# Performance work log

Measured on AMD Instinct MI355X. Metric: run time of the kernel, lower is better.

The kernel has to match this reference:

```python
import jax, jax.numpy as jnp
import numpy as np

B, S, D, H = 4, 2048, 1024, 16
HD = D // H          # head_dim = 64; per-head scale = sqrt(HD) as in source
FF = 4096
EPS = 1e-5


def _layernorm(x, g, b):
    m = jnp.mean(x, axis=-1, keepdims=True)
    v = jnp.mean(jnp.square(x - m), axis=-1, keepdims=True)
    return (x - m) * jax.lax.rsqrt(v + EPS) * g + b


def setup_inputs() -> dict:
    key = jax.random.key(0)
    ks = jax.random.split(key, 10)
    std = 0.02
    return {
        "x": jax.random.normal(ks[0], (B, S, D), jnp.float32),
        "wq": jax.random.normal(ks[1], (H, D, HD), jnp.float32) * std,
        "bq": jnp.zeros((H, HD), jnp.float32),
        "wk": jax.random.normal(ks[2], (H, D, HD), jnp.float32) * std,
        "bk": jnp.zeros((H, HD), jnp.float32),
        "wv": jax.random.normal(ks[3], (H, D, HD), jnp.float32) * std,
        "bv": jnp.zeros((H, HD), jnp.float32),
        "wo": jax.random.normal(ks[4], (D, D), jnp.float32) * std,
        "bo": jnp.zeros((D,), jnp.float32),
        "w1": jax.random.normal(ks[5], (D, FF), jnp.float32) * std,
        "b1": jnp.zeros((FF,), jnp.float32),
        "w2": jax.random.normal(ks[6], (FF, D), jnp.float32) * std,
        "b2": jnp.zeros((D,), jnp.float32),
        "g1": jnp.ones((D,), jnp.float32),
        "beta1": jnp.zeros((D,), jnp.float32),
        "g2": jnp.ones((D,), jnp.float32),
        "beta2": jnp.zeros((D,), jnp.float32),
    }


def reference(x, wq, bq, wk, bk, wv, bv, wo, bo, w1, b1, w2, b2, g1, beta1, g2, beta2):
    # Per-head Q/K/V projections (stacked over heads) -> [B,H,S,HD]
    q = jnp.einsum('bsd,hdf->bhsf', x, wq) + bq[None, :, None, :]
    k = jnp.einsum('bsd,hdf->bhsf', x, wk) + bk[None, :, None, :]
    v = jnp.einsum('bsd,hdf->bhsf', x, wv) + bv[None, :, None, :]

    scale = jnp.sqrt(jnp.asarray(HD, jnp.float32))
    att = jnp.einsum('bhqf,bhkf->bhqk', q, k) / scale  # [B,H,S,S]
    causal = jnp.tril(jnp.ones((S, S), dtype=bool))
    att = jnp.where(causal[None, None], att, -jnp.inf)
    p = jax.nn.softmax(att, axis=-1)
    o = jnp.einsum('bhqk,bhkf->bhqf', p, v)            # [B,H,S,HD]
    o = o.transpose(0, 2, 1, 3).reshape(B, S, D)       # concat heads
    attn_out = o @ wo + bo

    h = _layernorm(x + attn_out, g1, beta1)            # post-LN, dropout=0 (eval)
    ff = jax.nn.gelu(h @ w1 + b1, approximate=False) @ w2 + b2
    return _layernorm(h + ff, g2, beta2)
```

## Files before the change

### kernel.cpp

```cpp
#include <hip/hip_runtime.h>
#include <hip/hip_bf16.h>
#include <math.h>

typedef __bf16 bf16x8 __attribute__((ext_vector_type(8)));
typedef float floatx4 __attribute__((ext_vector_type(4)));
typedef unsigned short ushort8 __attribute__((ext_vector_type(8)));
typedef unsigned short ushort4v __attribute__((ext_vector_type(4)));

__device__ __forceinline__ unsigned short f2bs(float f){
  union { float f; unsigned u; } v; v.f = f;
  unsigned r = v.u + 0x7fffu + ((v.u >> 16) & 1u);
  return (unsigned short)(r >> 16);
}

__device__ __forceinline__ unsigned pk2(float a, float b){
  union { __hip_bfloat162 h; unsigned u; } cv;
  cv.h = __float22bfloat162_rn(make_float2(a, b));
  return cv.u;
}

__device__ __forceinline__ void gl_lds16(const void* g, void* l){
  __builtin_amdgcn_global_load_lds(
      (const __attribute__((address_space(1))) void*)g,
      (__attribute__((address_space(3))) void*)l,
      16, 0, 0);
}

__global__ __launch_bounds__(256) void cvt_x(const float* __restrict__ x,
                                             unsigned short* __restrict__ o){
  const int i = (blockIdx.x*256 + threadIdx.x)*4;
  const float4 v = *(const float4*)(x + i);
  ushort4v u = { f2bs(v.x), f2bs(v.y), f2bs(v.z), f2bs(v.w) };
  *(ushort4v*)(o + i) = u;
}

__global__ __launch_bounds__(256) void transpose_pack(const float* __restrict__ src,
                                                      unsigned short* __restrict__ dst,
                                                      int R, int C){
  __shared__ float tile[32][65];
  const int r0 = blockIdx.y*32, c0 = blockIdx.x*64;
  const int t = threadIdx.x;
  {
    const int r = t >> 3, cc = (t & 7)*8;
    const float* p = src + (size_t)(r0+r)*C + c0 + cc;
    const float4 v0 = *(const float4*)p;
    const float4 v1 = *(const float4*)(p+4);
    tile[r][cc+0]=v0.x; tile[r][cc+1]=v0.y; tile[r][cc+2]=v0.z; tile[r][cc+3]=v0.w;
    tile[r][cc+4]=v1.x; tile[r][cc+5]=v1.y; tile[r][cc+6]=v1.z; tile[r][cc+7]=v1.w;
  }
  __syncthreads();
  const int f = t >> 2, rr = (t & 3)*8;
  ushort8 u;
  #pragma unroll
  for (int j=0;j<8;j++) u[j] = f2bs(tile[rr+j][f]);
  *(ushort8*)(dst + (size_t)(c0+f)*R + r0 + rr) = u;
}

__global__ __launch_bounds__(256) void pack_qkv(const float* __restrict__ wq,
                                                const float* __restrict__ wk,
                                                const float* __restrict__ wv,
                                                const float* __restrict__ bq,
                                                const float* __restrict__ bk,
                                                const float* __restrict__ bv,
                                                unsigned short* __restrict__ Wt,
                                                float* __restrict__ Bc){
  __shared__ float tile[32][65];
  const int dt = blockIdx.x, h = blockIdx.y, sel = blockIdx.z;
  const float* src = (sel==0 ? wq : (sel==1 ? wk : wv)) + (size_t)h*65536;
  const int t = threadIdx.x, d0 = dt*32;
  {
    const int r = t >> 3, cc = (t & 7)*8;
    const float* p = src + (size_t)(d0+r)*64 + cc;
    const float4 v0 = *(const float4*)p;
    const float4 v1 = *(const float4*)(p+4);
    tile[r][cc+0]=v0.x; tile[r][cc+1]=v0.y; tile[r][cc+2]=v0.z; tile[r][cc+3]=v0.w;
    tile[r][cc+4]=v1.x; tile[r][cc+5]=v1.y; tile[r][cc+6]=v1.z; tile[r][cc+7]=v1.w;
  }
  __syncthreads();
  const int f = t >> 2, rr = (t & 3)*8;
  ushort8 u;
  #pragma unroll
  for (int j=0;j<8;j++) u[j] = f2bs(tile[rr+j][f]);
  const size_t n = (size_t)sel*1024 + h*64 + f;
  *(ushort8*)(Wt + n*1024 + d0 + rr) = u;
  if (dt==0 && t<64){
    const float* bs = (sel==0 ? bq : (sel==1 ? bk : bv)) + h*64;
    Bc[sel*1024 + h*64 + t] = bs[t];
  }
}

template<int MODE>
__global__ __launch_bounds__(256) void gemm_bt(const unsigned short* __restrict__ A,
                                               const unsigned short* __restrict__ Bt,
                                               const float* __restrict__ bias,
                                               void* __restrict__ out0,
                                               void* __restrict__ out1,
                                               void* __restrict__ out2,
                                               int M, int N, int K){
  __shared__ __align__(16) unsigned short As[128*64];
  __shared__ __align__(16) unsigned short Bs[128*64];
  const int tid = threadIdx.x;
  const int wave = tid >> 6, lane = tid & 63;
  const int quad = lane >> 4, l15 = lane & 15;
  const int lin = blockIdx.x;
  const int xcd = lin & 7, rest = lin >> 3;
  const int mloc = rest & 7, nt = rest >> 3;
  const int m0 = (xcd*8 + mloc) << 7, n0 = nt << 7;
  const int wr = (wave >> 1) << 6, wc = (wave & 1) << 6;

  floatx4 acc[4][4];
  #pragma unroll
  for (int i=0;i<4;i++)
    #pragma unroll
    for (int j=0;j<4;j++) acc[i][j] = (floatx4)0.0f;

  const unsigned short* gA[4];
  const unsigned short* gB[4];
  int ldsOff[4];
  #pragma unroll
  for (int r2=0;r2<4;r2++){
    const int slot = r2*256 + wave*64 + lane;
    const int row = slot >> 3, ch = slot & 7;
    const int col = (ch ^ (row & 7))*8;
    gA[r2] = A  + (size_t)(m0 + row)*K + col;
    gB[r2] = Bt + (size_t)(n0 + row)*K + col;
    ldsOff[r2] = slot*8;
  }
  const int cs0 = (quad ^ (l15 & 7))*8;
  const int cs1 = ((4 + quad) ^ (l15 & 7))*8;

  for (int k0 = 0; k0 < K; k0 += 64){
    #pragma unroll
    for (int r2=0;r2<4;r2++){
      gl_lds16(gA[r2] + k0, As + ldsOff[r2]);
      gl_lds16(gB[r2] + k0, Bs + ldsOff[r2]);
    }
    __syncthreads();
    #pragma unroll
    for (int ks=0;ks<2;ks++){
      const int cs = ks ? cs1 : cs0;
      bf16x8 af[4], bfv[4];
      #pragma unroll
      for (int t=0;t<4;t++){
        af[t]  = *(const bf16x8*)(As + (wr + t*16 + l15)*64 + cs);
        bfv[t] = *(const bf16x8*)(Bs + (wc + t*16 + l15)*64 + cs);
      }
      #pragma unroll
      for (int i=0;i<4;i++)
        #pragma unroll
        for (int j=0;j<4;j++)
          acc[i][j] = __builtin_amdgcn_mfma_f32_16x16x32_bf16(af[i], bfv[j], acc[i][j], 0,0,0);
    }
    __syncthreads();
  }

  #pragma unroll
  for (int i=0;i<4;i++){
    #pragma unroll
    for (int j=0;j<4;j++){
      const int col = n0 + wc + j*16 + l15;
      const float bsv = bias[col];
      if (MODE == 3 && col >= 2048){
        const int n = col - 2048, h = n >> 6, fidx = n & 63;
        const int rowb = m0 + wr + i*16 + quad*4;
        const int b = rowb >> 11, s = rowb & 2047;
        float v0 = acc[i][j][0] + bsv, v1 = acc[i][j][1] + bsv;
        float v2 = acc[i][j][2] + bsv, v3 = acc[i][j][3] + bsv;
        uint2 pkd = make_uint2(pk2(v0, v1), pk2(v2, v3));
        *(uint2*)((unsigned short*)out2 + (size_t)(((b<<4) + h)*64 + fidx)*2048 + s) = pkd;
        continue;
      }
      #pragma unroll
      for (int r=0;r<4;r++){
        const int row = m0 + wr + i*16 + quad*4 + r;
        const float v = acc[i][j][r] + bsv;
        if (MODE == 1){
          ((float*)out0)[(size_t)row*N + col] = v;
        } else if (MODE == 2){
          const float u = 0.7978845608f*v*(1.0f + 0.044715f*v*v);
          const float e = __builtin_amdgcn_exp2f(u * 2.885390082f);
          const float th = 1.0f - 2.0f/(1.0f + e);
          const float gl = 0.5f*v*(1.0f + th);
          ((unsigned short*)out0)[(size_t)row*N + col] = f2bs(gl);
        } else {
          if (col < 1024){
            ((unsigned short*)out0)[(size_t)row*1024 + col] = f2bs(v*0.18033688011112042f);
          } else {
            ((unsigned short*)out1)[(size_t)row*1024 + (col-1024)] = f2bs(v);
          }
        }
      }
    }
  }
}

__global__ __launch_bounds__(256, 4) void attn(const unsigned short* __restrict__ Q,
                                               const unsigned short* __restrict__ Kg,
                                               const unsigned short* __restrict__ Vt,
                                               unsigned short* __restrict__ O){
  __shared__ __align__(16) unsigned short Ks[64*64];
  __shared__ __align__(16) unsigned short Vs[64*64];
  __shared__ __align__(16) unsigned short PT[4][16*68];

  const int qt_lo = blockIdx.x;
  const int qt_hi = 31 - qt_lo;
  const int bh = blockIdx.y;
  const int b = bh >> 4, h = bh & 15;
  const int tid = threadIdx.x, wave = tid >> 6, lane = tid & 63;
  const int quad = lane >> 4, l15 = lane & 15;

  const size_t qbase = (size_t)((b<<11) + (wave<<4) + l15)*1024 + (h<<6);
  bf16x8 qf_hi[2], qf_lo[2];
  qf_hi[0] = *(const bf16x8*)(Q + qbase + (size_t)(qt_hi<<6)*1024 + quad*8);
  qf_hi[1] = *(const bf16x8*)(Q + qbase + (size_t)(qt_hi<<6)*1024 + 32 + quad*8);
  qf_lo[0] = *(const bf16x8*)(Q + qbase + (size_t)(qt_lo<<6)*1024 + quad*8);
  qf_lo[1] = *(const bf16x8*)(Q + qbase + (size_t)(qt_lo<<6)*1024 + 32 + quad*8);

  floatx4 oa_hi[4], oa_lo[4];
  #pragma unroll
  for (int i=0;i<4;i++){ oa_hi[i] = (floatx4)0.0f; oa_lo[i] = (floatx4)0.0f; }
  float mi_hi = -3e38f, li_hi = 0.0f;
  float mi_lo = -3e38f, li_lo = 0.0f;

  const unsigned short* Kbh = Kg + ((size_t)(b<<11))*1024 + (h<<6);
  const unsigned short* Vbh = Vt + (size_t)bh*64*2048;
  unsigned short* Pw = &PT[wave][0];

  const int slot0 = wave*128 + lane;
  const int krow0 = slot0 >> 3, kc0 = (slot0 & 7) ^ (krow0 & 7);
  const int slot1 = slot0 + 64;
  const int krow1 = slot1 >> 3, kc1 = (slot1 & 7) ^ (krow1 & 7);

  auto tile_step = [&](const bf16x8* qf, floatx4* oa, float& mi, float& li, bool diag){
    floatx4 sa[4];
    #pragma unroll
    for (int tj=0;tj<4;tj++){
      sa[tj] = (floatx4)0.0f;
      #pragma unroll
      for (int ks=0;ks<2;ks++){
        const int n = tj*16 + l15;
        const int c = (ks*4 + quad) ^ (n & 7);
        const bf16x8 kf = *(const bf16x8*)(Ks + n*64 + c*8);
        sa[tj] = __builtin_amdgcn_mfma_f32_16x16x32_bf16(kf, qf[ks], sa[tj], 0,0,0);
      }
    }
    if (diag){
      const int qrow = (wave<<4) + l15;
      #pragma unroll
      for (int tj=0;tj<4;tj++)
        #pragma unroll
        for (int r=0;r<4;r++)
          if (tj*16 + quad*4 + r > qrow) sa[tj][r] = -1e30f;
    }
    float mx = fmaxf(fmaxf(fmaxf(sa[0][0],sa[0][1]),fmaxf(sa[0][2],sa[0][3])),
                     fmaxf(fmaxf(sa[1][0],sa[1][1]),fmaxf(sa[1][2],sa[1][3])));
    mx = fmaxf(mx, fmaxf(fmaxf(fmaxf(sa[2][0],sa[2][1]),fmaxf(sa[2][2],sa[2][3])),
                         fmaxf(fmaxf(sa[3][0],sa[3][1]),fmaxf(sa[3][2],sa[3][3]))));
    mx = fmaxf(mx, __shfl_xor(mx, 16, 64));
    mx = fmaxf(mx, __shfl_xor(mx, 32, 64));
    const float mn = fmaxf(mi, mx);
    const float al = __builtin_amdgcn_exp2f(mi - mn);
    float rs = 0.0f;
    #pragma unroll
    for (int tj=0;tj<4;tj++)
      #pragma unroll
      for (int r=0;r<4;r++){
        const float p = __builtin_amdgcn_exp2f(sa[tj][r] - mn);
        sa[tj][r] = p;
        rs += p;
      }
    rs += __shfl_xor(rs, 16, 64);
    rs += __shfl_xor(rs, 32, 64);
    li = li*al + rs;
    mi = mn;
    #pragma unroll
    for (int tn=0;tn<4;tn++) oa[tn] *= al;

    #pragma unroll
    for (int tj=0;tj<4;tj++){
      uint2 pkd = make_uint2(pk2(sa[tj][0], sa[tj][1]), pk2(sa[tj][2], sa[tj][3]));
      *(uint2*)(Pw + l15*68 + tj*16 + quad*4) = pkd;
    }
    #pragma unroll
    for (int ks2=0;ks2<2;ks2++){
      const bf16x8 pf = *(const bf16x8*)(Pw + l15*68 + ks2*32 + quad*8);
      #pragma unroll
      for (int tn=0;tn<4;tn++){
        const int n2 = tn*16 + l15;
        const int c = (ks2*4 + quad) ^ (n2 & 7);
        const bf16x8 vf = *(const bf16x8*)(Vs + n2*64 + c*8);
        oa[tn] = __builtin_amdgcn_mfma_f32_16x16x32_bf16(vf, pf, oa[tn], 0,0,0);
      }
    }
  };

  for (int kt = 0; kt <= qt_hi; ++kt){
    gl_lds16(Kbh + (size_t)((kt<<6) + krow0)*1024 + kc0*8, Ks + wave*1024);
    gl_lds16(Kbh + (size_t)((kt<<6) + krow1)*1024 + kc1*8, Ks + wave*1024 + 512);
    gl_lds16(Vbh + (size_t)krow0*2048 + (kt<<6) + kc0*8, Vs + wave*1024);
    gl_lds16(Vbh + (size_t)krow1*2048 + (kt<<6) + kc1*8, Vs + wave*1024 + 512);
    __syncthreads();

    tile_step(qf_hi, oa_hi, mi_hi, li_hi, kt == qt_hi);
    if (kt <= qt_lo)
      tile_step(qf_lo, oa_lo, mi_lo, li_lo, kt == qt_lo);

    __syncthreads();
  }

  {
    const float inv = 1.0f / li_hi;
    unsigned short* Orow = O + (size_t)((b<<11) + (qt_hi<<6) + (wave<<4) + l15)*1024 + (h<<6);
    #pragma unroll
    for (int tn=0;tn<4;tn++){
      uint2 pkd = make_uint2(pk2(oa_hi[tn][0]*inv, oa_hi[tn][1]*inv),
                             pk2(oa_hi[tn][2]*inv, oa_hi[tn][3]*inv));
      *(uint2*)(Orow + tn*16 + quad*4) = pkd;
    }
  }
  {
    const float inv = 1.0f / li_lo;
    unsigned short* Orow = O + (size_t)((b<<11) + (qt_lo<<6) + (wave<<4) + l15)*1024 + (h<<6);
    #pragma unroll
    for (int tn=0;tn<4;tn++){
      uint2 pkd = make_uint2(pk2(oa_lo[tn][0]*inv, oa_lo[tn][1]*inv),
                             pk2(oa_lo[tn][2]*inv, oa_lo[tn][3]*inv));
      *(uint2*)(Orow + tn*16 + quad*4) = pkd;
    }
  }
}

__global__ __launch_bounds__(256) void ln_res(const float* __restrict__ a,
                                              const float* __restrict__ bsrc,
                                              const float* __restrict__ g,
                                              const float* __restrict__ be,
                                              float* __restrict__ of,
                                              unsigned short* __restrict__ ob){
  __shared__ float red1[4], red2[4];
  const int row = blockIdx.x, t = threadIdx.x;
  const int wave = t >> 6, lane = t & 63;
  const float4 va = *(const float4*)(a + (size_t)row*1024 + t*4);
  const float4 vb = *(const float4*)(bsrc + (size_t)row*1024 + t*4);
  float xs[4] = {va.x+vb.x, va.y+vb.y, va.z+vb.z, va.w+vb.w};
  float s = xs[0]+xs[1]+xs[2]+xs[3];
  #pragma unroll
  for (int d=1; d<64; d<<=1) s += __shfl_xor(s, d, 64);
  if (lane==0) red1[wave] = s;
  __syncthreads();
  const float mean = (red1[0]+red1[1]+red1[2]+red1[3]) * (1.0f/1024.0f);
  float vsum = 0.0f;
  #pragma unroll
  for (int i=0;i<4;i++){ const float d = xs[i]-mean; vsum += d*d; }
  #pragma unroll
  for (int d=1; d<64; d<<=1) vsum += __shfl_xor(vsum, d, 64);
  if (lane==0) red2[wave] = vsum;
  __syncthreads();
  const float var = (red2[0]+red2[1]+red2[2]+red2[3]) * (1.0f/1024.0f);
  const float rs = rsqrtf(var + 1e-5f);
  const float4 gg = *(const float4*)(g + t*4);
  const float4 bb = *(const float4*)(be + t*4);
  float y[4];
  y[0] = (xs[0]-mean)*rs*gg.x + bb.x;
  y[1] = (xs[1]-mean)*rs*gg.y + bb.y;
  y[2] = (xs[2]-mean)*rs*gg.z + bb.z;
  y[3] = (xs[3]-mean)*rs*gg.w + bb.w;
  if (of){
    float4 o4; o4.x=y[0]; o4.y=y[1]; o4.z=y[2]; o4.w=y[3];
    *(float4*)(of + (size_t)row*1024 + t*4) = o4;
  }
  if (ob){
    ushort4v u = { f2bs(y[0]), f2bs(y[1]), f2bs(y[2]), f2bs(y[3]) };
    *(ushort4v*)(ob + (size_t)row*1024 + t*4) = u;
  }
}

extern "C" void kernel_launch(void* const* d_in, const int* in_sizes, int n_in,
                              void* d_out, int out_size, void* d_ws, size_t ws_size,
                              hipStream_t stream){
  (void)in_sizes; (void)n_in; (void)out_size; (void)ws_size;
  const float* x  = (const float*)d_in[0];
  const float* wq = (const float*)d_in[1];
  const float* bq = (const float*)d_in[2];
  const float* wk = (const float*)d_in[3];
  const float* bk = (const float*)d_in[4];
  const float* wv = (const float*)d_in[5];
  const float* bv = (const float*)d_in[6];
  const float* wo = (const float*)d_in[7];
  const float* bo = (const float*)d_in[8];
  const float* w1 = (const float*)d_in[9];
  const float* b1 = (const float*)d_in[10];
  const float* w2 = (const float*)d_in[11];
  const float* b2 = (const float*)d_in[12];
  const float* g1 = (const float*)d_in[13];
  const float* be1= (const float*)d_in[14];
  const float* g2 = (const float*)d_in[15];
  const float* be2= (const float*)d_in[16];
  float* out = (float*)d_out;

  char* ws = (char*)d_ws;
  size_t off = 0;
  auto take = [&](size_t bytes)->char*{
    char* p = ws + off; off += (bytes + 255) & ~(size_t)255; return p;
  };
  unsigned short* Xb  = (unsigned short*)take(8192UL*1024*2);
  unsigned short* Qb  = (unsigned short*)take(8192UL*1024*2);
  unsigned short* Kb  = (unsigned short*)take(8192UL*1024*2);
  unsigned short* Vtb = (unsigned short*)take(8192UL*1024*2);
  unsigned short* Ob  = (unsigned short*)take(8192UL*1024*2);
  unsigned short* Midb= Qb;
  unsigned short* Wqkv= (unsigned short*)take(3072UL*1024*2);
  float*          Bqkv= (float*)take(3072UL*4);
  unsigned short* Wot = (unsigned short*)take(1024UL*1024*2);
  unsigned short* W1t = (unsigned short*)take(4096UL*1024*2);
  unsigned short* W2t = (unsigned short*)take(1024UL*4096*2);
  float*          C1  = (float*)take(8192UL*1024*4);
  float*          Ff  = C1;
  float*          Hf  = (float*)take(8192UL*1024*4);
  unsigned short* Hb  = (unsigned short*)take(8192UL*1024*2);

  cvt_x<<<8192, 256, 0, stream>>>(x, Xb);
  pack_qkv<<<dim3(32,16,3), 256, 0, stream>>>(wq, wk, wv, bq, bk, bv, Wqkv, Bqkv);
  transpose_pack<<<dim3(16,32),  256, 0, stream>>>(wo, Wot, 1024, 1024);
  transpose_pack<<<dim3(64,32),  256, 0, stream>>>(w1, W1t, 1024, 4096);
  transpose_pack<<<dim3(16,128), 256, 0, stream>>>(w2, W2t, 4096, 1024);

  gemm_bt<3><<<64*24, 256, 0, stream>>>(Xb, Wqkv, Bqkv, Qb, Kb, Vtb, 8192, 3072, 1024);

  attn<<<dim3(16,64), 256, 0, stream>>>(Qb, Kb, Vtb, Ob);

  gemm_bt<1><<<64*8, 256, 0, stream>>>(Ob, Wot, bo, C1, nullptr, nullptr, 8192, 1024, 1024);
  ln_res<<<8192, 256, 0, stream>>>(x, C1, g1, be1, Hf, Hb);

  gemm_bt<2><<<64*32, 256, 0, stream>>>(Hb, W1t, b1, Midb, nullptr, nullptr, 8192, 4096, 1024);
  gemm_bt<1><<<64*8, 256, 0, stream>>>(Midb, W2t, b2, Ff, nullptr, nullptr, 8192, 1024, 4096);
  ln_res<<<8192, 256, 0, stream>>>(Hf, Ff, g2, be2, out, nullptr);
}
```

Measured before the change: 602.0 us.

## Swap GEMM operand roles and double-buffer LDS with K-step 32

```diff
diff --git a/kernel.cpp b/kernel.cpp
--- a/kernel.cpp
+++ b/kernel.cpp
@@ -90,22 +90,22 @@
 }
 
 template<int MODE>
-__global__ __launch_bounds__(256) void gemm_bt(const unsigned short* __restrict__ A,
+__global__ __launch_bounds__(256) void gemm_tn(const unsigned short* __restrict__ A,
                                                const unsigned short* __restrict__ Bt,
                                                const float* __restrict__ bias,
                                                void* __restrict__ out0,
                                                void* __restrict__ out1,
                                                void* __restrict__ out2,
-                                               int M, int N, int K){
-  __shared__ __align__(16) unsigned short As[128*64];
-  __shared__ __align__(16) unsigned short Bs[128*64];
+                                               int K, int OW){
+  __shared__ __align__(16) unsigned short As[2][128*32];
+  __shared__ __align__(16) unsigned short Bs[2][128*32];
   const int tid = threadIdx.x;
   const int wave = tid >> 6, lane = tid & 63;
   const int quad = lane >> 4, l15 = lane & 15;
   const int lin = blockIdx.x;
   const int xcd = lin & 7, rest = lin >> 3;
-  const int mloc = rest & 7, nt = rest >> 3;
-  const int m0 = (xcd*8 + mloc) << 7, n0 = nt << 7;
+  const int nt = xcd*8 + (rest & 7), mt = rest >> 3;
+  const int m0 = mt << 7, n0 = nt << 7;
   const int wr = (wave >> 1) << 6, wc = (wave & 1) << 6;
 
   floatx4 acc[4][4];
@@ -114,80 +114,99 @@
     #pragma unroll
     for (int j=0;j<4;j++) acc[i][j] = (floatx4)0.0f;
 
-  const unsigned short* gA[4];
-  const unsigned short* gB[4];
-  int ldsOff[4];
-  #pragma unroll
-  for (int r2=0;r2<4;r2++){
-    const int slot = r2*256 + wave*64 + lane;
-    const int row = slot >> 3, ch = slot & 7;
-    const int col = (ch ^ (row & 7))*8;
-    gA[r2] = A  + (size_t)(m0 + row)*K + col;
-    gB[r2] = Bt + (size_t)(n0 + row)*K + col;
-    ldsOff[r2] = slot*8;
-  }
-  const int cs0 = (quad ^ (l15 & 7))*8;
-  const int cs1 = ((4 + quad) ^ (l15 & 7))*8;
-
-  for (int k0 = 0; k0 < K; k0 += 64){
-    #pragma unroll
-    for (int r2=0;r2<4;r2++){
-      gl_lds16(gA[r2] + k0, As + ldsOff[r2]);
-      gl_lds16(gB[r2] + k0, Bs + ldsOff[r2]);
-    }
+  const unsigned short* gA[2];
+  const unsigned short* gB[2];
+  int lofs[2];
+  #pragma unroll
+  for (int r2=0;r2<2;r2++){
+    const int slot = r2*256 + tid;
+    const int rp = slot >> 3, rem = slot & 7;
+    const int row = rp*2 + (rem >> 2);
+    const int kc = (rem & 3) ^ (rp & 3);
+    gA[r2] = A  + (size_t)(m0 + row)*K + kc*8;
+    gB[r2] = Bt + (size_t)(n0 + row)*K + kc*8;
+    lofs[r2] = slot*8;
+  }
+  int aofs[4], bofs[4];
+  #pragma unroll
+  for (int t=0;t<4;t++){
+    const int ra = wr + t*16 + l15;
+    aofs[t] = (ra>>1)*64 + (ra&1)*32 + ((quad ^ ((ra>>1)&3))<<3);
+    const int rb = wc + t*16 + l15;
+    bofs[t] = (rb>>1)*64 + (rb&1)*32 + ((quad ^ ((rb>>1)&3))<<3);
+  }
+
+  #pragma unroll
+  for (int r2=0;r2<2;r2++){
+    gl_lds16(gA[r2], &As[0][lofs[r2]]);
+    gl_lds16(gB[r2], &Bs[0][lofs[r2]]);
+  }
+
+  int buf = 0;
+  for (int k0 = 0; k0 < K; k0 += 32, buf ^= 1){
     __syncthreads();
-    #pragma unroll
-    for (int ks=0;ks<2;ks++){
-      const int cs = ks ? cs1 : cs0;
-      bf16x8 af[4], bfv[4];
-      #pragma unroll
-      for (int t=0;t<4;t++){
-        af[t]  = *(const bf16x8*)(As + (wr + t*16 + l15)*64 + cs);
-        bfv[t] = *(const bf16x8*)(Bs + (wc + t*16 + l15)*64 + cs);
+    if (k0 + 32 < K){
+      #pragma unroll
+      for (int r2=0;r2<2;r2++){
+        gl_lds16(gA[r2] + k0 + 32, &As[buf^1][lofs[r2]]);
+        gl_lds16(gB[r2] + k0 + 32, &Bs[buf^1][lofs[r2]]);
       }
-      #pragma unroll
-      for (int i=0;i<4;i++)
+    }
+    bf16x8 af[4], bfv[4];
+    #pragma unroll
+    for (int t=0;t<4;t++){
+      af[t]  = *(const bf16x8*)(&As[buf][aofs[t]]);
+      bfv[t] = *(const bf16x8*)(&Bs[buf][bofs[t]]);
+    }
+    #pragma unroll
+    for (int i=0;i<4;i++)
+      #pragma unroll
+      for (int j=0;j<4;j++)
+        acc[i][j] = __builtin_amdgcn_mfma_f32_16x16x32_bf16(af[i], bfv[j], acc[i][j], 0,0,0);
+  }
+
+  #pragma unroll
+  for (int i=0;i<4;i++){
+    const int row0 = m0 + wr + i*16 + quad*4;
+    const float4 b4 = *(const float4*)(bias + row0);
+    #pragma unroll
+    for (int j=0;j<4;j++){
+      const int tok = n0 + wc + j*16 + l15;
+      float v0 = acc[i][j][0] + b4.x;
+      float v1 = acc[i][j][1] + b4.y;
+      float v2 = acc[i][j][2] + b4.z;
+      float v3 = acc[i][j][3] + b4.w;
+      if (MODE == 1){
+        float4 o4; o4.x=v0; o4.y=v1; o4.z=v2; o4.w=v3;
+        *(float4*)((float*)out0 + (size_t)tok*OW + row0) = o4;
+      } else if (MODE == 2){
         #pragma unroll
-        for (int j=0;j<4;j++)
-          acc[i][j] = __builtin_amdgcn_mfma_f32_16x16x32_bf16(af[i], bfv[j], acc[i][j], 0,0,0);
-    }
-    __syncthreads();
-  }
-
-  #pragma unroll
-  for (int i=0;i<4;i++){
-    #pragma unroll
-    for (int j=0;j<4;j++){
-      const int col = n0 + wc + j*16 + l15;
-      const float bsv = bias[col];
-      if (MODE == 3 && col >= 2048){
-        const int n = col - 2048, h = n >> 6, fidx = n & 63;
-        const int rowb = m0 + wr + i*16 + quad*4;
-        const int b = rowb >> 11, s = rowb & 2047;
-        float v0 = acc[i][j][0] + bsv, v1 = acc[i][j][1] + bsv;
-        float v2 = acc[i][j][2] + bsv, v3 = acc[i][j][3] + bsv;
-        uint2 pkd = make_uint2(pk2(v0, v1), pk2(v2, v3));
-        *(uint2*)((unsigned short*)out2 + (size_t)(((b<<4) + h)*64 + fidx)*2048 + s) = pkd;
-        continue;
-      }
-      #pragma unroll
-      for (int r=0;r<4;r++){
-        const int row = m0 + wr + i*16 + quad*4 + r;
-        const float v = acc[i][j][r] + bsv;
-        if (MODE == 1){
-          ((float*)out0)[(size_t)row*N + col] = v;
-        } else if (MODE == 2){
+        for (int r=0;r<1;r++){}
+        float vv[4] = {v0,v1,v2,v3};
+        #pragma unroll
+        for (int r=0;r<4;r++){
+          const float v = vv[r];
           const float u = 0.7978845608f*v*(1.0f + 0.044715f*v*v);
           const float e = __builtin_amdgcn_exp2f(u * 2.885390082f);
-          const float th = 1.0f - 2.0f/(1.0f + e);
-          const float gl = 0.5f*v*(1.0f + th);
-          ((unsigned short*)out0)[(size_t)row*N + col] = f2bs(gl);
+          vv[r] = 0.5f*v*(1.0f + (1.0f - 2.0f/(1.0f + e)));
+        }
+        uint2 pkd = make_uint2(pk2(vv[0], vv[1]), pk2(vv[2], vv[3]));
+        *(uint2*)((unsigned short*)out0 + (size_t)tok*4096 + row0) = pkd;
+      } else {
+        if (row0 < 1024){
+          const float s = 0.18033688011112042f;
+          uint2 pkd = make_uint2(pk2(v0*s, v1*s), pk2(v2*s, v3*s));
+          *(uint2*)((unsigned short*)out0 + (size_t)tok*1024 + row0) = pkd;
+        } else if (row0 < 2048){
+          uint2 pkd = make_uint2(pk2(v0, v1), pk2(v2, v3));
+          *(uint2*)((unsigned short*)out1 + (size_t)tok*1024 + (row0-1024)) = pkd;
         } else {
-          if (col < 1024){
-            ((unsigned short*)out0)[(size_t)row*1024 + col] = f2bs(v*0.18033688011112042f);
-          } else {
-            ((unsigned short*)out1)[(size_t)row*1024 + (col-1024)] = f2bs(v);
-          }
+          const int rr = row0 - 2048, h = rr >> 6, f0 = rr & 63;
+          const int b = tok >> 11, s = tok & 2047;
+          unsigned short* vb = (unsigned short*)out2 +
+              (size_t)(((b<<4) + h)*64 + f0)*2048 + s;
+          vb[0] = f2bs(v0); vb[2048] = f2bs(v1);
+          vb[4096] = f2bs(v2); vb[6144] = f2bs(v3);
         }
       }
     }
@@ -424,14 +443,14 @@
   transpose_pack<<<dim3(64,32),  256, 0, stream>>>(w1, W1t, 1024, 4096);
   transpose_pack<<<dim3(16,128), 256, 0, stream>>>(w2, W2t, 4096, 1024);
 
-  gemm_bt<3><<<64*24, 256, 0, stream>>>(Xb, Wqkv, Bqkv, Qb, Kb, Vtb, 8192, 3072, 1024);
+  gemm_tn<3><<<64*24, 256, 0, stream>>>(Wqkv, Xb, Bqkv, Qb, Kb, Vtb, 1024, 0);
 
   attn<<<dim3(16,64), 256, 0, stream>>>(Qb, Kb, Vtb, Ob);
 
-  gemm_bt<1><<<64*8, 256, 0, stream>>>(Ob, Wot, bo, C1, nullptr, nullptr, 8192, 1024, 1024);
+  gemm_tn<1><<<64*8, 256, 0, stream>>>(Wot, Ob, bo, C1, nullptr, nullptr, 1024, 1024);
   ln_res<<<8192, 256, 0, stream>>>(x, C1, g1, be1, Hf, Hb);
 
-  gemm_bt<2><<<64*32, 256, 0, stream>>>(Hb, W1t, b1, Midb, nullptr, nullptr, 8192, 4096, 1024);
-  gemm_bt<1><<<64*8, 256, 0, stream>>>(Midb, W2t, b2, Ff, nullptr, nullptr, 8192, 1024, 4096);
+  gemm_tn<2><<<64*32, 256, 0, stream>>>(W1t, Hb, b1, Midb, nullptr, nullptr, 1024, 4096);
+  gemm_tn<1><<<64*8, 256, 0, stream>>>(W2t, Midb, b2, Ff, nullptr, nullptr, 4096, 1024);
   ln_res<<<8192, 256, 0, stream>>>(Hf, Ff, g2, be2, out, nullptr);
 }
```

Result: slower. 631.4 us (+4.9%).
